# Kernel optimization log

Hardware: AMD Instinct MI355X
Metric: run time of the kernel (lower is better)

The kernel has to match this reference:

```python
import jax, jax.numpy as jnp
import numpy as np

D_MODEL = 1024
N_HEADS = 16
D_K = D_MODEL // N_HEADS


def setup_inputs() -> dict:
    key = jax.random.key(0)
    ks = jax.random.split(key, 9)
    s = 1.0 / np.sqrt(D_MODEL)
    def lin(kw, kb):
        W = jax.random.uniform(kw, (D_MODEL, D_MODEL), jnp.float32, -s, s)
        b = jax.random.uniform(kb, (D_MODEL,), jnp.float32, -s, s)
        return W, b
    wq, bq = lin(ks[0], ks[1])
    wk, bk = lin(ks[2], ks[3])
    wv, bv = lin(ks[4], ks[5])
    wo, bo = lin(ks[6], ks[7])
    x = jax.random.normal(ks[8], (2, 2048, D_MODEL), jnp.float32)
    return {"x": x, "wq": wq, "bq": bq, "wk": wk, "bk": bk,
            "wv": wv, "bv": bv, "wo": wo, "bo": bo}


def reference(x, wq, bq, wk, bk, wv, bv, wo, bo):
    B, S, D = x.shape
    scale = 1.0 / np.sqrt(D_K)
    # projections (torch Linear: y = x W^T + b); W stored as [in,out] here
    q = x @ wq + bq
    k = x @ wk + bk
    v = x @ wv + bv
    # [B, H, S, d_k]
    q = q.reshape(B, S, N_HEADS, D_K).transpose(0, 2, 1, 3)
    k = k.reshape(B, S, N_HEADS, D_K).transpose(0, 2, 1, 3)
    v = v.reshape(B, S, N_HEADS, D_K).transpose(0, 2, 1, 3)
    scores = jnp.einsum('bhqd,bhkd->bhqk', q, k) * scale
    attn = jax.nn.softmax(scores, axis=-1)
    out = jnp.einsum('bhqk,bhkd->bhqd', attn, v)
    out = out.transpose(0, 2, 1, 3).reshape(B, S, D)
    return out @ wo + bo
```

## Files before the change

kernel.cpp:

```cpp
#include <hip/hip_runtime.h>
#include <hip/hip_bf16.h>
#include <math.h>

typedef __bf16 bf16x8 __attribute__((ext_vector_type(8)));
typedef unsigned short u16x8 __attribute__((ext_vector_type(8)));
typedef unsigned short u16x4 __attribute__((ext_vector_type(4)));
typedef float f32x4 __attribute__((ext_vector_type(4)));
typedef unsigned int u32x4 __attribute__((ext_vector_type(4)));
typedef unsigned int u32x2 __attribute__((ext_vector_type(2)));
typedef unsigned short u16;

__device__ __forceinline__ u16 f2bf(float f) {
    unsigned int x = __float_as_uint(f);
    x += 0x7fffu + ((x >> 16) & 1u);
    return (u16)(x >> 16);
}
__device__ __forceinline__ void glds16(const void* g, void* l) {
    __builtin_amdgcn_global_load_lds(
        (const __attribute__((address_space(1))) void*)g,
        (__attribute__((address_space(3))) void*)l, 16, 0, 0);
}
__device__ __forceinline__ void swap_half(unsigned& a, unsigned& b) {
    u32x2 t = __builtin_amdgcn_permlane32_swap(a, b, false, false);
    t = __builtin_amdgcn_permlane16_swap(t[0], t[1], false, false);
    a = t[0]; b = t[1];
}

__global__ __launch_bounds__(256) void prep(const float* __restrict__ W0, const float* __restrict__ W1,
                                            const float* __restrict__ W2, const float* __restrict__ W3,
                                            const float* __restrict__ X,
                                            u16* __restrict__ Wt, u16* __restrict__ Xb) {
    int z = blockIdx.z;
    if (z >= 4) {
        int row = (z - 4) * 1024 + blockIdx.y * 32 + blockIdx.x;
        const float* src = X + (size_t)row * 1024 + threadIdx.x * 4;
        f32x4 v = *(const f32x4*)src;
        u16x4 o; o[0] = f2bf(v[0]); o[1] = f2bf(v[1]); o[2] = f2bf(v[2]); o[3] = f2bf(v[3]);
        *(u16x4*)&Xb[(size_t)row * 1024 + threadIdx.x * 4] = o;
        return;
    }
    __shared__ float T[32][33];
    const float* W = (z == 0) ? W0 : ((z == 1) ? W1 : ((z == 2) ? W2 : W3));
    u16* dst = Wt + (size_t)z * 1024 * 1024;
    int k0 = blockIdx.y * 32, n0 = blockIdx.x * 32;
    int x = threadIdx.x & 31, y0 = threadIdx.x >> 5;
#pragma unroll
    for (int i = 0; i < 4; i++) {
        int y = y0 + i * 8;
        T[y][x] = W[(size_t)(k0 + y) * 1024 + n0 + x];
    }
    __syncthreads();
#pragma unroll
    for (int i = 0; i < 4; i++) {
        int y = y0 + i * 8;
        dst[(size_t)(n0 + y) * 1024 + k0 + x] = f2bf(T[x][y]);
    }
}

__global__ __launch_bounds__(512, 2) void gemm256(
    const u16* __restrict__ Bt,
    const float* __restrict__ b0, const float* __restrict__ b1, const float* __restrict__ b2,
    const u16* __restrict__ A, u16* __restrict__ C, u16* __restrict__ Vt)
{
    __shared__ __align__(16) u16 As[2][256 * 64];
    __shared__ __align__(16) u16 Bs[2][256 * 64];
    int tid = threadIdx.x;
    int lane = tid & 63, l15 = lane & 15, quad = lane >> 4;
    int wid = tid >> 6;
    int wm = wid >> 2, wn = wid & 3;
    int m0 = blockIdx.y * 256, n0 = blockIdx.x * 256;
    int sel = n0 >> 10;
    const float* bias = (sel == 0) ? b0 : ((sel == 1) ? b1 : b2);

    f32x4 acc[8][4];
#pragma unroll
    for (int i = 0; i < 8; i++)
#pragma unroll
        for (int j = 0; j < 4; j++) { f32x4 z = {0.f, 0.f, 0.f, 0.f}; acc[i][j] = z; }

    int rr = lane >> 3;
    int cc = (lane & 7) ^ rr;
    int fs7 = l15 & 7;
    const u16* abase = A  + (size_t)m0 * 1024;
    const u16* bbase = Bt + (size_t)n0 * 1024;

    auto stage = [&](int kt, int hp, int buf) {
        const u16* gsrc = (hp < 2) ? abase : bbase;
        u16* ldst = (hp < 2) ? As[buf] : Bs[buf];
        int k0 = kt * 64;
        int hbase = (hp & 1) * 128;
#pragma unroll
        for (int inst = 0; inst < 2; inst++) {
            int r0 = hbase + wid * 16 + inst * 8;
            glds16(&gsrc[(size_t)(r0 + rr) * 1024 + k0 + cc * 8], &ldst[r0 * 64]);
        }
    };

#pragma unroll
    for (int hp = 0; hp < 4; hp++) stage(0, hp, 0);

#pragma unroll 2
    for (int it = 0; it < 16; ++it) {
        int c = it & 1;
        if (it < 15) {
            stage(it + 1, 0, c ^ 1);
            asm volatile("s_waitcnt vmcnt(2)");
        } else {
            asm volatile("s_waitcnt vmcnt(0)");
        }
        __builtin_amdgcn_s_barrier();
        bf16x8 bfr[4][2];
#pragma unroll
        for (int nt = 0; nt < 4; nt++)
#pragma unroll
            for (int h = 0; h < 2; h++)
                bfr[nt][h] = *(const bf16x8*)&Bs[c][(wn * 64 + nt * 16 + l15) * 64 +
                                                    ((((h << 2) | quad) ^ fs7) * 8)];
        {
            bf16x8 af[2][2];
#pragma unroll
            for (int m = 0; m < 2; m++)
#pragma unroll
                for (int h = 0; h < 2; h++)
                    af[m][h] = *(const bf16x8*)&As[c][(wm * 128 + m * 16 + l15) * 64 +
                                                      ((((h << 2) | quad) ^ fs7) * 8)];
            asm volatile("s_waitcnt lgkmcnt(0)");
            __builtin_amdgcn_sched_barrier(0);
            __builtin_amdgcn_s_setprio(1);
#pragma unroll
            for (int m = 0; m < 2; m++)
#pragma unroll
                for (int nt = 0; nt < 4; nt++)
#pragma unroll
                    for (int h = 0; h < 2; h++)
                        acc[m][nt] = __builtin_amdgcn_mfma_f32_16x16x32_bf16(
                            af[m][h], bfr[nt][h], acc[m][nt], 0, 0, 0);
            __builtin_amdgcn_s_setprio(0);
            __builtin_amdgcn_s_barrier();
        }
#pragma unroll
        for (int p = 1; p < 4; p++) {
            bf16x8 af[2][2];
#pragma unroll
            for (int m = 0; m < 2; m++)
#pragma unroll
                for (int h = 0; h < 2; h++)
                    af[m][h] = *(const bf16x8*)&As[c][(wm * 128 + (p * 2 + m) * 16 + l15) * 64 +
                                                      ((((h << 2) | quad) ^ fs7) * 8)];
            if (it < 15) stage(it + 1, p, c ^ 1);
            __builtin_amdgcn_s_barrier();
            asm volatile("s_waitcnt lgkmcnt(0)");
            __builtin_amdgcn_sched_barrier(0);
            __builtin_amdgcn_s_setprio(1);
#pragma unroll
            for (int m = 0; m < 2; m++)
#pragma unroll
                for (int nt = 0; nt < 4; nt++)
#pragma unroll
                    for (int h = 0; h < 2; h++)
                        acc[p * 2 + m][nt] = __builtin_amdgcn_mfma_f32_16x16x32_bf16(
                            af[m][h], bfr[nt][h], acc[p * 2 + m][nt], 0, 0, 0);
            __builtin_amdgcn_s_setprio(0);
            __builtin_amdgcn_s_barrier();
        }
    }

    if (sel == 2) {
        int b = m0 >> 11;
#pragma unroll
        for (int mt = 0; mt < 8; mt++) {
            int gr = m0 + wm * 128 + mt * 16 + quad * 4;
            int s = gr & 2047;
#pragma unroll
            for (int nt = 0; nt < 4; nt++) {
                int gcl = (n0 & 1023) + wn * 64 + nt * 16 + l15;
                float bb = bias[gcl];
                u16x4 pk;
#pragma unroll
                for (int r = 0; r < 4; r++) pk[r] = f2bf(acc[mt][nt][r] + bb);
                *(u16x4*)&Vt[(size_t)((b * 16 + (gcl >> 6)) * 64 + (gcl & 63)) * 2048 + s] = pk;
            }
        }
        return;
    }
    float qs = (sel == 0) ? 0.18033688011112f : 1.0f;
#pragma unroll
    for (int mt = 0; mt < 8; mt++) {
        int gr = m0 + wm * 128 + mt * 16 + quad * 4;
#pragma unroll
        for (int nt = 0; nt < 4; nt++) {
            int gc = n0 + wn * 64 + nt * 16 + l15;
            float bb = bias[gc & 1023];
#pragma unroll
            for (int r = 0; r < 4; r++)
                C[(size_t)(gr + r) * 3072 + gc] = f2bf((acc[mt][nt][r] + bb) * qs);
        }
    }
}

template <bool OF32, bool VSPLIT>
__global__ __launch_bounds__(256) void gemm(
    const u16* __restrict__ Bt,
    const float* __restrict__ b0, const float* __restrict__ b1, const float* __restrict__ b2,
    const u16* __restrict__ A, void* __restrict__ Cptr, u16* __restrict__ Vt, int Ntot)
{
    __shared__ __align__(16) u16 As[128 * 32];
    __shared__ __align__(16) u16 Bs[128 * 32];
    int tid = threadIdx.x;
    int lane = tid & 63, l15 = lane & 15, quad = lane >> 4;
    int wid = tid >> 6, wm = wid >> 1, wn = wid & 1;
    int m0 = blockIdx.y * 128, n0 = blockIdx.x * 128;
    int sel = n0 >> 10;
    const float* bias = (sel == 0) ? b0 : ((sel == 1) ? b1 : b2);

    f32x4 acc[4][4];
#pragma unroll
    for (int i = 0; i < 4; i++)
#pragma unroll
        for (int j = 0; j < 4; j++) { f32x4 z = {0.f, 0.f, 0.f, 0.f}; acc[i][j] = z; }

    int rr = lane >> 2;
    int cc = (lane & 3) ^ ((rr >> 1) & 3);
    const u16* abase = A  + (size_t)m0 * 1024;
    const u16* bbase = Bt + (size_t)n0 * 1024;
    int fsw = (l15 >> 1) & 3;

    for (int k0 = 0; k0 < 1024; k0 += 32) {
#pragma unroll
        for (int inst = 0; inst < 2; inst++) {
            int r0 = wid * 32 + inst * 16;
            glds16(&abase[(size_t)(r0 + rr) * 1024 + k0 + cc * 8], &As[r0 * 32]);
            glds16(&bbase[(size_t)(r0 + rr) * 1024 + k0 + cc * 8], &Bs[r0 * 32]);
        }
        __syncthreads();
        bf16x8 af[4], bf[4];
#pragma unroll
        for (int mt = 0; mt < 4; mt++)
            af[mt] = *(const bf16x8*)&As[(wm * 64 + mt * 16 + l15) * 32 + ((quad ^ fsw) * 8)];
#pragma unroll
        for (int nt = 0; nt < 4; nt++)
            bf[nt] = *(const bf16x8*)&Bs[(wn * 64 + nt * 16 + l15) * 32 + ((quad ^ fsw) * 8)];
#pragma unroll
        for (int mt = 0; mt < 4; mt++)
#pragma unroll
            for (int nt = 0; nt < 4; nt++)
                acc[mt][nt] = __builtin_amdgcn_mfma_f32_16x16x32_bf16(af[mt], bf[nt], acc[mt][nt], 0, 0, 0);
        __syncthreads();
    }
    if (VSPLIT && sel == 2) {
        int b = m0 >> 11;
#pragma unroll
        for (int mt = 0; mt < 4; mt++) {
            int gr = m0 + wm * 64 + mt * 16 + quad * 4;
            int s = gr & 2047;
#pragma unroll
            for (int nt = 0; nt < 4; nt++) {
                int gcl = (n0 & 1023) + wn * 64 + nt * 16 + l15;
                float bb = bias[gcl];
                u16x4 pk;
#pragma unroll
                for (int r = 0; r < 4; r++) pk[r] = f2bf(acc[mt][nt][r] + bb);
                *(u16x4*)&Vt[(size_t)((b * 16 + (gcl >> 6)) * 64 + (gcl & 63)) * 2048 + s] = pk;
            }
        }
        return;
    }
    float qs = (VSPLIT && sel == 0) ? 0.18033688011112f : 1.0f;
#pragma unroll
    for (int mt = 0; mt < 4; mt++) {
        int gr = m0 + wm * 64 + mt * 16 + quad * 4;
#pragma unroll
        for (int nt = 0; nt < 4; nt++) {
            int gc = n0 + wn * 64 + nt * 16 + l15;
            float bb = bias[gc & 1023];
#pragma unroll
            for (int r = 0; r < 4; r++) {
                float v = (acc[mt][nt][r] + bb) * qs;
                if (OF32) ((float*)Cptr)[(size_t)(gr + r) * Ntot + gc] = v;
                else      ((u16*)Cptr)[(size_t)(gr + r) * Ntot + gc] = f2bf(v);
            }
        }
    }
}

__global__ __launch_bounds__(256, 2) void attn(const u16* __restrict__ QKV,
                                               const u16* __restrict__ Vt,
                                               u16* __restrict__ O)
{
    __shared__ __align__(16) u16 Ks[2][64 * 64];
    __shared__ __align__(16) u16 Vs[2][64 * 64];
    const int S = 2048, DQ = 3072;
    int tid = threadIdx.x, wid = tid >> 6, lane = tid & 63;
    int l15 = lane & 15, quad = lane >> 4;
    int qt = blockIdx.x, h = blockIdx.y, b = blockIdx.z;
    const u16* base = QKV + (size_t)b * S * DQ + h * 64;
    const u16* Kb = base + 1024;
    const u16* Vtb = Vt + (size_t)((b * 16 + h) * 64) * 2048;
    int q0 = qt * 128 + wid * 32;

    bf16x8 qA0 = *(const bf16x8*)&base[(size_t)(q0 + l15) * DQ + quad * 8];
    bf16x8 qA1 = *(const bf16x8*)&base[(size_t)(q0 + l15) * DQ + 32 + quad * 8];
    bf16x8 qB0 = *(const bf16x8*)&base[(size_t)(q0 + 16 + l15) * DQ + quad * 8];
    bf16x8 qB1 = *(const bf16x8*)&base[(size_t)(q0 + 16 + l15) * DQ + 32 + quad * 8];

    f32x4 oA[4], oB[4];
#pragma unroll
    for (int i = 0; i < 4; i++) { f32x4 z = {0.f, 0.f, 0.f, 0.f}; oA[i] = z; oB[i] = z; }
    float psA = 0.f, psB = 0.f;

    int rr = lane >> 3;
    int cc = (lane & 7) ^ rr;
    int fs7 = l15 & 7;

    auto stage = [&](int it, int bsel) {
        int kv0 = it << 6;
#pragma unroll
        for (int inst = 0; inst < 2; inst++) {
            int r0 = wid * 16 + inst * 8;
            glds16(&Kb[(size_t)(kv0 + r0 + rr) * DQ + cc * 8], &Ks[bsel][r0 * 64]);
            glds16(&Vtb[(size_t)(r0 + rr) * 2048 + kv0 + cc * 8], &Vs[bsel][r0 * 64]);
        }
    };

    stage(0, 0);
#pragma unroll 2
    for (int it = 0; it < 32; ++it) {
        int cur = it & 1;
        if (it < 31) {
            stage(it + 1, cur ^ 1);
            asm volatile("s_waitcnt vmcnt(4)\n\ts_barrier" ::: "memory");
        } else {
            asm volatile("s_waitcnt vmcnt(0)\n\ts_barrier" ::: "memory");
        }

        f32x4 sA[4], sB[4];
#pragma unroll
        for (int t = 0; t < 4; t++) { f32x4 z = {0.f, 0.f, 0.f, 0.f}; sA[t] = z; sB[t] = z; }
#pragma unroll
        for (int t = 0; t < 4; t++) {
            bf16x8 kfa = *(const bf16x8*)&Ks[cur][(t * 16 + l15) * 64 + ((quad ^ fs7) * 8)];
            bf16x8 kfb = *(const bf16x8*)&Ks[cur][(t * 16 + l15) * 64 + (((quad + 4) ^ fs7) * 8)];
            sA[t] = __builtin_amdgcn_mfma_f32_16x16x32_bf16(kfa, qA0, sA[t], 0, 0, 0);
            sA[t] = __builtin_amdgcn_mfma_f32_16x16x32_bf16(kfb, qA1, sA[t], 0, 0, 0);
            sB[t] = __builtin_amdgcn_mfma_f32_16x16x32_bf16(kfa, qB0, sB[t], 0, 0, 0);
            sB[t] = __builtin_amdgcn_mfma_f32_16x16x32_bf16(kfb, qB1, sB[t], 0, 0, 0);
        }

        unsigned wA[4][2], wB[4][2];
#pragma unroll
        for (int t = 0; t < 4; t++) {
            float a0 = __builtin_amdgcn_exp2f(sA[t][0]);
            float a1 = __builtin_amdgcn_exp2f(sA[t][1]);
            float a2 = __builtin_amdgcn_exp2f(sA[t][2]);
            float a3 = __builtin_amdgcn_exp2f(sA[t][3]);
            psA += (a0 + a1) + (a2 + a3);
            asm("v_cvt_pk_bf16_f32 %0, %1, %2" : "=v"(wA[t][0]) : "v"(a0), "v"(a1));
            asm("v_cvt_pk_bf16_f32 %0, %1, %2" : "=v"(wA[t][1]) : "v"(a2), "v"(a3));
            float b0_ = __builtin_amdgcn_exp2f(sB[t][0]);
            float b1_ = __builtin_amdgcn_exp2f(sB[t][1]);
            float b2_ = __builtin_amdgcn_exp2f(sB[t][2]);
            float b3_ = __builtin_amdgcn_exp2f(sB[t][3]);
            psB += (b0_ + b1_) + (b2_ + b3_);
            asm("v_cvt_pk_bf16_f32 %0, %1, %2" : "=v"(wB[t][0]) : "v"(b0_), "v"(b1_));
            asm("v_cvt_pk_bf16_f32 %0, %1, %2" : "=v"(wB[t][1]) : "v"(b2_), "v"(b3_));
        }
        unsigned a0 = wA[0][0], a2 = wA[1][0]; swap_half(a0, a2);
        unsigned a1 = wA[0][1], a3 = wA[1][1]; swap_half(a1, a3);
        unsigned c0 = wA[2][0], c2 = wA[3][0]; swap_half(c0, c2);
        unsigned c1 = wA[2][1], c3 = wA[3][1]; swap_half(c1, c3);
        u32x4 pdA0 = {a0, a1, a2, a3};
        u32x4 pdA1 = {c0, c1, c2, c3};
        bf16x8 pfA0 = *(bf16x8*)&pdA0;
        bf16x8 pfA1 = *(bf16x8*)&pdA1;
        unsigned d0 = wB[0][0], d2 = wB[1][0]; swap_half(d0, d2);
        unsigned d1 = wB[0][1], d3 = wB[1][1]; swap_half(d1, d3);
        unsigned e0 = wB[2][0], e2 = wB[3][0]; swap_half(e0, e2);
        unsigned e1 = wB[2][1], e3 = wB[3][1]; swap_half(e1, e3);
        u32x4 pdB0 = {d0, d1, d2, d3};
        u32x4 pdB1 = {e0, e1, e2, e3};
        bf16x8 pfB0 = *(bf16x8*)&pdB0;
        bf16x8 pfB1 = *(bf16x8*)&pdB1;

#pragma unroll
        for (int dt = 0; dt < 4; dt++) {
            bf16x8 vfa = *(const bf16x8*)&Vs[cur][(dt * 16 + l15) * 64 + ((quad ^ fs7) * 8)];
            bf16x8 vfb = *(const bf16x8*)&Vs[cur][(dt * 16 + l15) * 64 + (((quad + 4) ^ fs7) * 8)];
            oA[dt] = __builtin_amdgcn_mfma_f32_16x16x32_bf16(pfA0, vfa, oA[dt], 0, 0, 0);
            oA[dt] = __builtin_amdgcn_mfma_f32_16x16x32_bf16(pfA1, vfb, oA[dt], 0, 0, 0);
            oB[dt] = __builtin_amdgcn_mfma_f32_16x16x32_bf16(pfB0, vfa, oB[dt], 0, 0, 0);
            oB[dt] = __builtin_amdgcn_mfma_f32_16x16x32_bf16(pfB1, vfb, oB[dt], 0, 0, 0);
        }
        asm volatile("s_barrier" ::: "memory");
    }

    psA += __shfl_xor(psA, 16);
    psA += __shfl_xor(psA, 32);
    psB += __shfl_xor(psB, 16);
    psB += __shfl_xor(psB, 32);
#pragma unroll
    for (int r = 0; r < 4; r++) {
        float invA = 1.0f / __shfl(psA, quad * 4 + r);
        size_t rowA = (size_t)(b * S + q0 + quad * 4 + r);
#pragma unroll
        for (int dt = 0; dt < 4; dt++)
            O[rowA * 1024 + h * 64 + dt * 16 + l15] = f2bf(oA[dt][r] * invA);
        float invB = 1.0f / __shfl(psB, quad * 4 + r);
        size_t rowB = rowA + 16;
#pragma unroll
        for (int dt = 0; dt < 4; dt++)
            O[rowB * 1024 + h * 64 + dt * 16 + l15] = f2bf(oB[dt][r] * invB);
    }
}

extern "C" void kernel_launch(void* const* d_in, const int* in_sizes, int n_in,
                              void* d_out, int out_size, void* d_ws, size_t ws_size,
                              hipStream_t stream) {
    const float* x  = (const float*)d_in[0];
    const float* wq = (const float*)d_in[1];
    const float* bq = (const float*)d_in[2];
    const float* wk = (const float*)d_in[3];
    const float* bk = (const float*)d_in[4];
    const float* wv = (const float*)d_in[5];
    const float* bv = (const float*)d_in[6];
    const float* wo = (const float*)d_in[7];
    const float* bo = (const float*)d_in[8];
    float* out = (float*)d_out;

    u16* qkv  = (u16*)d_ws;
    u16* obuf = qkv  + (size_t)4096 * 3072;
    u16* vt   = obuf + (size_t)4096 * 1024;
    u16* wt   = vt   + (size_t)2048 * 2048;
    u16* xb   = wt   + (size_t)4 * 1024 * 1024;

    dim3 tb(256);
    prep<<<dim3(32, 32, 8), tb, 0, stream>>>(wq, wk, wv, wo, x, wt, xb);
    gemm256<<<dim3(12, 16), dim3(512), 0, stream>>>(wt, bq, bk, bv, xb, qkv, vt);
    attn<<<dim3(16, 16, 2), tb, 0, stream>>>(qkv, vt, obuf);
    gemm<true, false><<<dim3(8, 32), tb, 0, stream>>>(wt + (size_t)3 * 1024 * 1024,
                                                      bo, bo, bo, obuf, out, (u16*)nullptr, 1024);
}
```

Before: 195.0 us.

## Deepen attention K/V pipeline, remap blocks across XCDs, prefetch LDS fragments

The attention kernel now uses a 4-slot K/V LDS ring with two tiles prefetched ahead, so the trailing barrier can be dropped and global loads have more time to land. It also loads all K and V fragments from LDS at the start of each iteration and raises wave priority around the MFMA blocks. The grid is flattened and remapped so that all query tiles of the same (batch, head) land on the same XCD, which is meant to improve L2 reuse of K/V. In exchange, LDS use doubles to 64KB per block, which may reduce occupancy, and register pressure goes up.

```diff
diff --git a/kernel.cpp b/kernel.cpp
--- a/kernel.cpp
+++ b/kernel.cpp
@@ -287,12 +287,17 @@
                                                const u16* __restrict__ Vt,
                                                u16* __restrict__ O)
 {
-    __shared__ __align__(16) u16 Ks[2][64 * 64];
-    __shared__ __align__(16) u16 Vs[2][64 * 64];
+    __shared__ __align__(16) u16 Ks[4][64 * 64];
+    __shared__ __align__(16) u16 Vs[4][64 * 64];
     const int S = 2048, DQ = 3072;
     int tid = threadIdx.x, wid = tid >> 6, lane = tid & 63;
     int l15 = lane & 15, quad = lane >> 4;
-    int qt = blockIdx.x, h = blockIdx.y, b = blockIdx.z;
+    int lin = blockIdx.x;
+    int xcd = lin & 7;
+    int rest = lin >> 3;
+    int qt = rest & 15;
+    int g = xcd + 8 * (rest >> 4);
+    int h = g & 15, b = g >> 4;
     const u16* base = QKV + (size_t)b * S * DQ + h * 64;
     const u16* Kb = base + 1024;
     const u16* Vtb = Vt + (size_t)((b * 16 + h) * 64) * 2048;
@@ -323,28 +328,45 @@
     };
 
     stage(0, 0);
-#pragma unroll 2
+    stage(1, 1);
     for (int it = 0; it < 32; ++it) {
-        int cur = it & 1;
-        if (it < 31) {
-            stage(it + 1, cur ^ 1);
-            asm volatile("s_waitcnt vmcnt(4)\n\ts_barrier" ::: "memory");
+        int cb = it & 3;
+        if (it < 30) {
+            stage(it + 2, (it + 2) & 3);
+            asm volatile("s_waitcnt vmcnt(8)");
+        } else if (it == 30) {
+            asm volatile("s_waitcnt vmcnt(4)");
         } else {
-            asm volatile("s_waitcnt vmcnt(0)\n\ts_barrier" ::: "memory");
+            asm volatile("s_waitcnt vmcnt(0)");
+        }
+        __builtin_amdgcn_s_barrier();
+
+        const u16* Kc = &Ks[cb][0];
+        const u16* Vc = &Vs[cb][0];
+        bf16x8 kfa[4], kfb[4], vfa[4], vfb[4];
+#pragma unroll
+        for (int t = 0; t < 4; t++) {
+            kfa[t] = *(const bf16x8*)&Kc[(t * 16 + l15) * 64 + ((quad ^ fs7) * 8)];
+            kfb[t] = *(const bf16x8*)&Kc[(t * 16 + l15) * 64 + (((quad + 4) ^ fs7) * 8)];
+        }
+#pragma unroll
+        for (int dt = 0; dt < 4; dt++) {
+            vfa[dt] = *(const bf16x8*)&Vc[(dt * 16 + l15) * 64 + ((quad ^ fs7) * 8)];
+            vfb[dt] = *(const bf16x8*)&Vc[(dt * 16 + l15) * 64 + (((quad + 4) ^ fs7) * 8)];
         }
 
         f32x4 sA[4], sB[4];
 #pragma unroll
         for (int t = 0; t < 4; t++) { f32x4 z = {0.f, 0.f, 0.f, 0.f}; sA[t] = z; sB[t] = z; }
+        __builtin_amdgcn_s_setprio(1);
 #pragma unroll
         for (int t = 0; t < 4; t++) {
-            bf16x8 kfa = *(const bf16x8*)&Ks[cur][(t * 16 + l15) * 64 + ((quad ^ fs7) * 8)];
-            bf16x8 kfb = *(const bf16x8*)&Ks[cur][(t * 16 + l15) * 64 + (((quad + 4) ^ fs7) * 8)];
-            sA[t] = __builtin_amdgcn_mfma_f32_16x16x32_bf16(kfa, qA0, sA[t], 0, 0, 0);
-            sA[t] = __builtin_amdgcn_mfma_f32_16x16x32_bf16(kfb, qA1, sA[t], 0, 0, 0);
-            sB[t] = __builtin_amdgcn_mfma_f32_16x16x32_bf16(kfa, qB0, sB[t], 0, 0, 0);
-            sB[t] = __builtin_amdgcn_mfma_f32_16x16x32_bf16(kfb, qB1, sB[t], 0, 0, 0);
-        }
+            sA[t] = __builtin_amdgcn_mfma_f32_16x16x32_bf16(kfa[t], qA0, sA[t], 0, 0, 0);
+            sA[t] = __builtin_amdgcn_mfma_f32_16x16x32_bf16(kfb[t], qA1, sA[t], 0, 0, 0);
+            sB[t] = __builtin_amdgcn_mfma_f32_16x16x32_bf16(kfa[t], qB0, sB[t], 0, 0, 0);
+            sB[t] = __builtin_amdgcn_mfma_f32_16x16x32_bf16(kfb[t], qB1, sB[t], 0, 0, 0);
+        }
+        __builtin_amdgcn_s_setprio(0);
 
         unsigned wA[4][2], wB[4][2];
 #pragma unroll
@@ -381,16 +403,15 @@
         bf16x8 pfB0 = *(bf16x8*)&pdB0;
         bf16x8 pfB1 = *(bf16x8*)&pdB1;
 
+        __builtin_amdgcn_s_setprio(1);
 #pragma unroll
         for (int dt = 0; dt < 4; dt++) {
-            bf16x8 vfa = *(const bf16x8*)&Vs[cur][(dt * 16 + l15) * 64 + ((quad ^ fs7) * 8)];
-            bf16x8 vfb = *(const bf16x8*)&Vs[cur][(dt * 16 + l15) * 64 + (((quad + 4) ^ fs7) * 8)];
-            oA[dt] = __builtin_amdgcn_mfma_f32_16x16x32_bf16(pfA0, vfa, oA[dt], 0, 0, 0);
-            oA[dt] = __builtin_amdgcn_mfma_f32_16x16x32_bf16(pfA1, vfb, oA[dt], 0, 0, 0);
-            oB[dt] = __builtin_amdgcn_mfma_f32_16x16x32_bf16(pfB0, vfa, oB[dt], 0, 0, 0);
-            oB[dt] = __builtin_amdgcn_mfma_f32_16x16x32_bf16(pfB1, vfb, oB[dt], 0, 0, 0);
-        }
-        asm volatile("s_barrier" ::: "memory");
+            oA[dt] = __builtin_amdgcn_mfma_f32_16x16x32_bf16(pfA0, vfa[dt], oA[dt], 0, 0, 0);
+            oA[dt] = __builtin_amdgcn_mfma_f32_16x16x32_bf16(pfA1, vfb[dt], oA[dt], 0, 0, 0);
+            oB[dt] = __builtin_amdgcn_mfma_f32_16x16x32_bf16(pfB0, vfa[dt], oB[dt], 0, 0, 0);
+            oB[dt] = __builtin_amdgcn_mfma_f32_16x16x32_bf16(pfB1, vfb[dt], oB[dt], 0, 0, 0);
+        }
+        __builtin_amdgcn_s_setprio(0);
     }
 
     psA += __shfl_xor(psA, 16);
@@ -435,7 +456,7 @@
     dim3 tb(256);
     prep<<<dim3(32, 32, 8), tb, 0, stream>>>(wq, wk, wv, wo, x, wt, xb);
     gemm256<<<dim3(12, 16), dim3(512), 0, stream>>>(wt, bq, bk, bv, xb, qkv, vt);
-    attn<<<dim3(16, 16, 2), tb, 0, stream>>>(qkv, vt, obuf);
+    attn<<<dim3(512), tb, 0, stream>>>(qkv, vt, obuf);
     gemm<true, false><<<dim3(8, 32), tb, 0, stream>>>(wt + (size_t)3 * 1024 * 1024,
                                                       bo, bo, bo, obuf, out, (u16*)nullptr, 1024);
 }
```

After: 193.2 us. About the same (-0.9%).
